# Kernel optimization log

Measured on AMD Instinct MI355X. Metric: run time of the kernel, lower is better.

## Reference

```python
import jax, jax.numpy as jnp
import numpy as np

N, K, H, W, C, P = 8, 16, 512, 512, 4, 200000


def setup_inputs() -> dict:
    key = jax.random.key(0)
    k1, k2, k3, k4, k5 = jax.random.split(key, 5)
    idx = jax.random.randint(k1, (N, K, H, W), 0, P, dtype=jnp.int32)
    # per-pixel valid-prefix lengths: indices are z-sorted, -1 fills the tail
    counts = jax.random.randint(k2, (N, 1, H, W), 0, K + 1, dtype=jnp.int32)
    valid = jnp.arange(K, dtype=jnp.int32)[None, :, None, None] < counts
    fragments = jnp.where(valid, idx, jnp.int32(-1))
    alphas = jax.random.uniform(k3, (N, K, H, W), dtype=jnp.float32)
    ptclds = jax.random.uniform(k4, (C, P), dtype=jnp.float32)
    background_color = jax.random.uniform(k5, (3,), dtype=jnp.float32)
    return dict(fragments=fragments, alphas=alphas, ptclds=ptclds,
                background_color=background_color)


def reference(fragments, alphas, ptclds, background_color):
    # --- alpha_composite: 'over' compositing front-to-back along K ---
    valid = fragments >= 0                       # (N,K,H,W)
    a = jnp.where(valid, alphas, 0.0)            # invalid slots contribute nothing
    # exclusive cumulative transmittance prod_{j<k} (1 - a_j)
    t = jnp.cumprod(1.0 - a, axis=1)
    trans = jnp.concatenate([jnp.ones_like(t[:, :1]), t[:, :-1]], axis=1)
    w = a * trans                                # per-sample blend weight (N,K,H,W)
    idx = jnp.maximum(fragments, 0)              # clamp -1 for the gather (weight is 0)
    gathered = ptclds.T[idx]                     # (N,K,H,W,C) irregular gather
    images = jnp.einsum('nkhwc,nkhw->nchw', gathered, w)  # (N,C,H,W)
    # --- _add_background_color_to_images (C == 4 branch) ---
    bg = jnp.concatenate([background_color, jnp.ones((1,), images.dtype)])  # rgba
    bg_mask = fragments[:, 0] < 0                # (N,H,W): pixels with no points
    images = jnp.where(bg_mask[:, None, :, :], bg[None, :, None, None], images)
    return images
```

## Files before the change

### kernel.cpp

```cpp
#include <hip/hip_runtime.h>


constexpr int N = 8, K = 16, H = 512, W = 512, C = 4, P = 200000;
constexpr int HW = H * W;
constexpr int NPIX = N * HW;

__global__ __launch_bounds__(256) void transpose_ptclds(
    const float* __restrict__ pt,
    float4* __restrict__ pt4)
{
    int p = blockIdx.x * blockDim.x + threadIdx.x;
    if (p < P) {
        pt4[p] = make_float4(pt[p], pt[P + p], pt[2 * P + p], pt[3 * P + p]);
    }
}

template <bool USE_T>
__global__ __launch_bounds__(256) void composite_kernel(
    const int* __restrict__ frag,
    const float* __restrict__ alpha,
    const float* __restrict__ pt,
    const float4* __restrict__ pt4,
    const float* __restrict__ bgc,
    float* __restrict__ out)
{
    int p = blockIdx.x * blockDim.x + threadIdx.x;
    if (p >= NPIX) return;
    int n = p >> 18;
    int hw = p & (HW - 1);

    const int* fp = frag + (size_t)n * K * HW + hw;
    const float* ap = alpha + (size_t)n * K * HW + hw;
    float* op = out + (size_t)n * C * HW + hw;

    int f0 = fp[0];
    if (f0 < 0) {
        op[0]      = bgc[0];
        op[HW]     = bgc[1];
        op[2 * HW] = bgc[2];
        op[3 * HW] = 1.0f;
        return;
    }

    int f[K];
    float av[K];
    f[0] = f0;
#pragma unroll
    for (int k = 1; k < K; ++k) f[k] = fp[(size_t)k * HW];
#pragma unroll
    for (int k = 0; k < K; ++k) av[k] = ap[(size_t)k * HW];

    float trans = 1.0f;
    float a0 = 0.0f, a1 = 0.0f, a2 = 0.0f, a3 = 0.0f;
#pragma unroll
    for (int k = 0; k < K; ++k) {
        bool valid = f[k] >= 0;
        float a = valid ? av[k] : 0.0f;
        float wgt = a * trans;
        trans *= (1.0f - a);
        if (valid) {
            if (USE_T) {
                float4 c = pt4[f[k]];
                a0 = fmaf(wgt, c.x, a0);
                a1 = fmaf(wgt, c.y, a1);
                a2 = fmaf(wgt, c.z, a2);
                a3 = fmaf(wgt, c.w, a3);
            } else {
                a0 = fmaf(wgt, pt[f[k]], a0);
                a1 = fmaf(wgt, pt[P + f[k]], a1);
                a2 = fmaf(wgt, pt[2 * P + f[k]], a2);
                a3 = fmaf(wgt, pt[3 * P + f[k]], a3);
            }
        }
    }

    op[0]      = a0;
    op[HW]     = a1;
    op[2 * HW] = a2;
    op[3 * HW] = a3;
}

extern "C" void kernel_launch(void* const* d_in, const int* in_sizes, int n_in,
                              void* d_out, int out_size, void* d_ws, size_t ws_size,
                              hipStream_t stream) {
    const int* frag    = (const int*)d_in[0];
    const float* alpha = (const float*)d_in[1];
    const float* pt    = (const float*)d_in[2];
    const float* bgc   = (const float*)d_in[3];
    float* out         = (float*)d_out;

    const bool use_t = ws_size >= (size_t)P * sizeof(float4);
    dim3 blk(256);
    if (use_t) {
        float4* pt4 = (float4*)d_ws;
        transpose_ptclds<<<(P + 255) / 256, blk, 0, stream>>>(pt, pt4);
        composite_kernel<true><<<(NPIX + 255) / 256, blk, 0, stream>>>(
            frag, alpha, pt, pt4, bgc, out);
    } else {
        composite_kernel<false><<<(NPIX + 255) / 256, blk, 0, stream>>>(
            frag, alpha, pt, nullptr, bgc, out);
    }
}
```

Before: 373.0 us.

## Issue all gathers unconditionally up front and use nontemporal streaming loads/stores

The composite kernel now loads all fragment indices and alphas with nontemporal loads, then issues all 16 float4 point gathers unconditionally, clamping -1 indices to 0, before the compositing loop. This exposes memory-level parallelism instead of branch-dependent gathers. The background early-exit becomes a select at the store, and the stores are nontemporal. The cost is extra gather traffic for invalid slots and background pixels, higher register pressure, and removal of the fallback when the workspace is too small.

```diff
diff --git a/kernel.cpp b/kernel.cpp
--- a/kernel.cpp
+++ b/kernel.cpp
@@ -15,11 +15,9 @@
     }
 }
 
-template <bool USE_T>
 __global__ __launch_bounds__(256) void composite_kernel(
     const int* __restrict__ frag,
     const float* __restrict__ alpha,
-    const float* __restrict__ pt,
     const float4* __restrict__ pt4,
     const float* __restrict__ bgc,
     float* __restrict__ out)
@@ -33,51 +31,42 @@
     const float* ap = alpha + (size_t)n * K * HW + hw;
     float* op = out + (size_t)n * C * HW + hw;
 
-    int f0 = fp[0];
-    if (f0 < 0) {
-        op[0]      = bgc[0];
-        op[HW]     = bgc[1];
-        op[2 * HW] = bgc[2];
-        op[3 * HW] = 1.0f;
-        return;
+    int f[K];
+#pragma unroll
+    for (int k = 0; k < K; ++k)
+        f[k] = __builtin_nontemporal_load(fp + (size_t)k * HW);
+
+    float av[K];
+#pragma unroll
+    for (int k = 0; k < K; ++k)
+        av[k] = __builtin_nontemporal_load(ap + (size_t)k * HW);
+
+    float4 c[K];
+#pragma unroll
+    for (int k = 0; k < K; ++k) {
+        int idx = f[k] >= 0 ? f[k] : 0;
+        c[k] = pt4[idx];
     }
-
-    int f[K];
-    float av[K];
-    f[0] = f0;
-#pragma unroll
-    for (int k = 1; k < K; ++k) f[k] = fp[(size_t)k * HW];
-#pragma unroll
-    for (int k = 0; k < K; ++k) av[k] = ap[(size_t)k * HW];
 
     float trans = 1.0f;
     float a0 = 0.0f, a1 = 0.0f, a2 = 0.0f, a3 = 0.0f;
 #pragma unroll
     for (int k = 0; k < K; ++k) {
-        bool valid = f[k] >= 0;
-        float a = valid ? av[k] : 0.0f;
+        float a = f[k] >= 0 ? av[k] : 0.0f;
         float wgt = a * trans;
         trans *= (1.0f - a);
-        if (valid) {
-            if (USE_T) {
-                float4 c = pt4[f[k]];
-                a0 = fmaf(wgt, c.x, a0);
-                a1 = fmaf(wgt, c.y, a1);
-                a2 = fmaf(wgt, c.z, a2);
-                a3 = fmaf(wgt, c.w, a3);
-            } else {
-                a0 = fmaf(wgt, pt[f[k]], a0);
-                a1 = fmaf(wgt, pt[P + f[k]], a1);
-                a2 = fmaf(wgt, pt[2 * P + f[k]], a2);
-                a3 = fmaf(wgt, pt[3 * P + f[k]], a3);
-            }
-        }
+        a0 = fmaf(wgt, c[k].x, a0);
+        a1 = fmaf(wgt, c[k].y, a1);
+        a2 = fmaf(wgt, c[k].z, a2);
+        a3 = fmaf(wgt, c[k].w, a3);
     }
 
-    op[0]      = a0;
-    op[HW]     = a1;
-    op[2 * HW] = a2;
-    op[3 * HW] = a3;
+    bool bg = f[0] < 0;
+    float b0 = bgc[0], b1 = bgc[1], b2 = bgc[2];
+    __builtin_nontemporal_store(bg ? b0 : a0, op);
+    __builtin_nontemporal_store(bg ? b1 : a1, op + HW);
+    __builtin_nontemporal_store(bg ? b2 : a2, op + 2 * HW);
+    __builtin_nontemporal_store(bg ? 1.0f : a3, op + 3 * HW);
 }
 
 extern "C" void kernel_launch(void* const* d_in, const int* in_sizes, int n_in,
@@ -89,15 +78,9 @@
     const float* bgc   = (const float*)d_in[3];
     float* out         = (float*)d_out;
 
-    const bool use_t = ws_size >= (size_t)P * sizeof(float4);
+    float4* pt4 = (float4*)d_ws;
     dim3 blk(256);
-    if (use_t) {
-        float4* pt4 = (float4*)d_ws;
-        transpose_ptclds<<<(P + 255) / 256, blk, 0, stream>>>(pt, pt4);
-        composite_kernel<true><<<(NPIX + 255) / 256, blk, 0, stream>>>(
-            frag, alpha, pt, pt4, bgc, out);
-    } else {
-        composite_kernel<false><<<(NPIX + 255) / 256, blk, 0, stream>>>(
-            frag, alpha, pt, nullptr, bgc, out);
-    }
+    transpose_ptclds<<<(P + 255) / 256, blk, 0, stream>>>(pt, pt4);
+    composite_kernel<<<(NPIX + 255) / 256, blk, 0, stream>>>(
+        frag, alpha, pt4, bgc, out);
 }
```

Result: faster. 354.9 us (-4.8%).
